# Kernel optimization log

Hardware: AMD Instinct MI355X
Metric: run time of the kernel (lower is better)

The kernel has to match this reference:

```python
import jax, jax.numpy as jnp
import numpy as np

L1, L2, N, C = 4096, 4096, 8, 3


def setup_inputs() -> dict:
    key = jax.random.key(0)
    k1, k2 = jax.random.split(key)
    coords1 = jax.random.uniform(k1, (L1, N, C), dtype=jnp.float32)
    coords2 = jax.random.uniform(k2, (L2, N, C), dtype=jnp.float32)
    return {"coords1": coords1, "coords2": coords2}


def reference(coords1, coords2):
    # coords1: [L1, N, C], coords2: [L2, N, C]
    l1, n, c = coords1.shape
    l2 = coords2.shape[0]
    # Batch-first layout, matching flatten_batch semantics (per-batch NN only)
    q = jnp.swapaxes(coords2, 0, 1)  # [N, L2, C] query points
    r = jnp.swapaxes(coords1, 0, 1)  # [N, L1, C] reference points
    # Squared euclidean distances per batch: [N, L2, L1]
    d2 = (
        jnp.sum(q * q, axis=-1)[:, :, None]
        + jnp.sum(r * r, axis=-1)[:, None, :]
        - 2.0 * jnp.einsum("nlc,nmc->nlm", q, r)
    )
    # tc.nearest returns global flat index; original does fmod(L1) to get the
    # per-batch index — argmin within each batch gives that directly.
    nearest = jnp.argmin(d2, axis=-1)  # [N, L2]
    clusters = nearest.T  # [L2, N]
    # torch.meshgrid(arange(L2), arange(N)) with 'ij' indexing; indices[-1] is
    # the batch index broadcast to [L2, N].
    batch_idx = jnp.broadcast_to(jnp.arange(n, dtype=jnp.int64 if False else jnp.int32), (l2, n))
    return (clusters.reshape(-1), batch_idx.reshape(-1))
```

## Files before the change

kernel.cpp:

```cpp
#include <hip/hip_runtime.h>
#include <float.h>


typedef float v2f __attribute__((ext_vector_type(2)));

constexpr int kL1 = 4096, kL2 = 4096, kN = 8;
constexpr int kChunk = 1024;
constexpr int kQPerBlock = 16;
constexpr int kQ = 4;

__device__ __forceinline__ v2f pk_mul(v2f a, v2f b) {
  v2f d; asm("v_pk_mul_f32 %0, %1, %2" : "=v"(d) : "v"(a), "v"(b)); return d;
}
__device__ __forceinline__ v2f pk_add(v2f a, v2f b) {
  v2f d; asm("v_pk_add_f32 %0, %1, %2" : "=v"(d) : "v"(a), "v"(b)); return d;
}
__device__ __forceinline__ v2f pk_fma(v2f a, v2f b, v2f c) {
  v2f d; asm("v_pk_fma_f32 %0, %1, %2, %3" : "=v"(d) : "v"(a), "v"(b), "v"(c)); return d;
}

__device__ __forceinline__ v2f dist2_pair(v2f qx, v2f qy, v2f qz, v2f qq,
                                          v2f rx, v2f ry, v2f rz, v2f rr, v2f n2) {
  const v2f s01 = pk_add(pk_mul(qx, rx), pk_mul(qy, ry));
  const v2f dot = pk_add(s01, pk_mul(qz, rz));
  const v2f A = pk_add(qq, rr);
  return pk_fma(dot, n2, A);
}

__global__ __launch_bounds__(256, 4)
void nearest_kernel(const float* __restrict__ c1, const float* __restrict__ c2,
                    int* __restrict__ out) {
#pragma clang fp contract(off)
  __shared__ float sRx[kChunk], sRy[kChunk], sRz[kChunk], sRr[kChunk];

  const int tid = threadIdx.x;
  const int n = blockIdx.y;
  const int wave = tid >> 6;
  const int lane = tid & 63;
  const int q0 = blockIdx.x * kQPerBlock + wave * kQ;

  float qxs[kQ], qys[kQ], qzs[kQ], qqs[kQ];
  v2f qx2[kQ], qy2[kQ], qz2[kQ], qq2[kQ];
#pragma unroll
  for (int i = 0; i < kQ; ++i) {
    const float* p = c2 + ((q0 + i) * kN + n) * 3;
    qxs[i] = p[0]; qys[i] = p[1]; qzs[i] = p[2];
    qqs[i] = __fadd_rn(__fadd_rn(__fmul_rn(qxs[i], qxs[i]), __fmul_rn(qys[i], qys[i])),
                       __fmul_rn(qzs[i], qzs[i]));
    qx2[i] = (v2f){qxs[i], qxs[i]};
    qy2[i] = (v2f){qys[i], qys[i]};
    qz2[i] = (v2f){qzs[i], qzs[i]};
    qq2[i] = (v2f){qqs[i], qqs[i]};
  }
  const v2f n2 = {-2.0f, -2.0f};

  float bd[kQ]; int bt[kQ];
#pragma unroll
  for (int i = 0; i < kQ; ++i) { bd[i] = FLT_MAX; bt[i] = 0; }

  for (int chunk = 0; chunk < kL1 / kChunk; ++chunk) {
    __syncthreads();

    {
      const int jb = chunk * kChunk + tid * 4;
      float x[4], y[4], z[4], w4[4];
#pragma unroll
      for (int k = 0; k < 4; ++k) {
        const float* p = c1 + ((jb + k) * kN + n) * 3;
        x[k] = p[0]; y[k] = p[1]; z[k] = p[2];
        w4[k] = __fadd_rn(__fadd_rn(__fmul_rn(x[k], x[k]), __fmul_rn(y[k], y[k])),
                          __fmul_rn(z[k], z[k]));
      }
      *reinterpret_cast<float4*>(&sRx[tid * 4]) = make_float4(x[0], x[1], x[2], x[3]);
      *reinterpret_cast<float4*>(&sRy[tid * 4]) = make_float4(y[0], y[1], y[2], y[3]);
      *reinterpret_cast<float4*>(&sRz[tid * 4]) = make_float4(z[0], z[1], z[2], z[3]);
      *reinterpret_cast<float4*>(&sRr[tid * 4]) = make_float4(w4[0], w4[1], w4[2], w4[3]);
    }
    __syncthreads();

#pragma unroll
    for (int t = 0; t < kChunk / 256; ++t) {
      const int tg = chunk * (kChunk / 256) + t;
      const int base = t * 256 + lane * 4;
      const float4 rx4 = *reinterpret_cast<const float4*>(&sRx[base]);
      const float4 ry4 = *reinterpret_cast<const float4*>(&sRy[base]);
      const float4 rz4 = *reinterpret_cast<const float4*>(&sRz[base]);
      const float4 rr4 = *reinterpret_cast<const float4*>(&sRr[base]);
      const v2f rx01 = {rx4.x, rx4.y}, rx23 = {rx4.z, rx4.w};
      const v2f ry01 = {ry4.x, ry4.y}, ry23 = {ry4.z, ry4.w};
      const v2f rz01 = {rz4.x, rz4.y}, rz23 = {rz4.z, rz4.w};
      const v2f rr01 = {rr4.x, rr4.y}, rr23 = {rr4.z, rr4.w};

#pragma unroll
      for (int i = 0; i < kQ; ++i) {
        const v2f d01 = dist2_pair(qx2[i], qy2[i], qz2[i], qq2[i],
                                   rx01, ry01, rz01, rr01, n2);
        const v2f d23 = dist2_pair(qx2[i], qy2[i], qz2[i], qq2[i],
                                   rx23, ry23, rz23, rr23, n2);
        const float old = bd[i];
        float m = fminf(fminf(d01.x, d01.y), old);
        m = fminf(fminf(d23.x, d23.y), m);
        bd[i] = m;
        if (m < old) bt[i] = tg;
      }
    }
  }

  int sel[kQ];
#pragma unroll
  for (int i = 0; i < kQ; ++i) sel[i] = bt[i] * 64 + lane;
#pragma unroll
  for (int m = 1; m <= 32; m <<= 1) {
#pragma unroll
    for (int i = 0; i < kQ; ++i) {
      const float od = __shfl_xor(bd[i], m);
      const int os = __shfl_xor(sel[i], m);
      if (od < bd[i] || (od == bd[i] && os < sel[i])) { bd[i] = od; sel[i] = os; }
    }
  }

#pragma unroll
  for (int i = 0; i < kQ; ++i) {
    if (lane == i) {
      const int j0 = sel[i] * 4;
      float best = FLT_MAX; int kk = 0;
#pragma unroll
      for (int k = 0; k < 4; ++k) {
        const float* p = c1 + ((j0 + k) * kN + n) * 3;
        const float r0 = p[0], r1 = p[1], r2 = p[2];
        const float rr = __fadd_rn(
            __fadd_rn(__fmul_rn(r0, r0), __fmul_rn(r1, r1)), __fmul_rn(r2, r2));
        const float dot = __fadd_rn(
            __fadd_rn(__fmul_rn(qxs[i], r0), __fmul_rn(qys[i], r1)),
            __fmul_rn(qzs[i], r2));
        const float dc = __fmaf_rn(-2.0f, dot, __fadd_rn(qqs[i], rr));
        if (dc < best) { best = dc; kk = k; }
      }
      out[(q0 + i) * kN + n] = j0 + kk;
      out[kL2 * kN + (q0 + i) * kN + n] = n;
    }
  }
}

extern "C" void kernel_launch(void* const* d_in, const int* in_sizes, int n_in,
                              void* d_out, int out_size, void* d_ws, size_t ws_size,
                              hipStream_t stream) {
  const float* c1 = (const float*)d_in[0];
  const float* c2 = (const float*)d_in[1];
  int* out = (int*)d_out;
  dim3 grid(kL2 / kQPerBlock, kN);
  nearest_kernel<<<grid, dim3(256), 0, stream>>>(c1, c2, out);
}
```

Baseline: 99.80 us.

## Precompute SoA reference layout in workspace and read it directly from global memory

Adds a pre-pass kernel that transposes coords1 into per-batch SoA arrays (x, y, z, |r|^2) in the workspace. The main kernel then streams these arrays from global/L2 with float4 loads, with no LDS staging or __syncthreads. Both paths also replace the inline-asm packed FP32 math with scalar arithmetic. This removes the strided AoS gathers that every block repeated and the block barriers, at the cost of an extra kernel launch, workspace traffic, and losing the packed-math throughput.

```diff
diff --git a/kernel.cpp b/kernel.cpp
--- a/kernel.cpp
+++ b/kernel.cpp
@@ -2,37 +2,126 @@
 #include <float.h>
 
 
-typedef float v2f __attribute__((ext_vector_type(2)));
-
 constexpr int kL1 = 4096, kL2 = 4096, kN = 8;
-constexpr int kChunk = 1024;
 constexpr int kQPerBlock = 16;
 constexpr int kQ = 4;
-
-__device__ __forceinline__ v2f pk_mul(v2f a, v2f b) {
-  v2f d; asm("v_pk_mul_f32 %0, %1, %2" : "=v"(d) : "v"(a), "v"(b)); return d;
-}
-__device__ __forceinline__ v2f pk_add(v2f a, v2f b) {
-  v2f d; asm("v_pk_add_f32 %0, %1, %2" : "=v"(d) : "v"(a), "v"(b)); return d;
-}
-__device__ __forceinline__ v2f pk_fma(v2f a, v2f b, v2f c) {
-  v2f d; asm("v_pk_fma_f32 %0, %1, %2, %3" : "=v"(d) : "v"(a), "v"(b), "v"(c)); return d;
-}
-
-__device__ __forceinline__ v2f dist2_pair(v2f qx, v2f qy, v2f qz, v2f qq,
-                                          v2f rx, v2f ry, v2f rz, v2f rr, v2f n2) {
-  const v2f s01 = pk_add(pk_mul(qx, rx), pk_mul(qy, ry));
-  const v2f dot = pk_add(s01, pk_mul(qz, rz));
-  const v2f A = pk_add(qq, rr);
-  return pk_fma(dot, n2, A);
+constexpr int kSoAFloats = kN * kL1;
+constexpr size_t kWsBytes = 4ull * kSoAFloats * sizeof(float);
+
+__global__ __launch_bounds__(256)
+void soa_kernel(const float* __restrict__ c1, float* __restrict__ ws) {
+#pragma clang fp contract(off)
+  const int t = blockIdx.x * 256 + threadIdx.x;
+  const int n = t & (kN - 1);
+  const int j = t >> 3;
+  const float* p = c1 + t * 3;
+  const float x = p[0], y = p[1], z = p[2];
+  const float rr = __fadd_rn(
+      __fadd_rn(__fmul_rn(x, x), __fmul_rn(y, y)), __fmul_rn(z, z));
+  const int o = n * kL1 + j;
+  ws[o] = x;
+  ws[kSoAFloats + o] = y;
+  ws[2 * kSoAFloats + o] = z;
+  ws[3 * kSoAFloats + o] = rr;
 }
 
 __global__ __launch_bounds__(256, 4)
-void nearest_kernel(const float* __restrict__ c1, const float* __restrict__ c2,
-                    int* __restrict__ out) {
+void nearest_soa_kernel(const float* __restrict__ ws, const float* __restrict__ c2,
+                        int* __restrict__ out) {
+#pragma clang fp contract(off)
+  const int n = blockIdx.y;
+  const int wave = threadIdx.x >> 6;
+  const int lane = threadIdx.x & 63;
+  const int q0 = blockIdx.x * kQPerBlock + wave * kQ;
+
+  const float* __restrict__ X = ws + n * kL1;
+  const float* __restrict__ Y = ws + kSoAFloats + n * kL1;
+  const float* __restrict__ Z = ws + 2 * kSoAFloats + n * kL1;
+  const float* __restrict__ RR = ws + 3 * kSoAFloats + n * kL1;
+
+  float qx[kQ], qy[kQ], qz[kQ], qq[kQ];
+#pragma unroll
+  for (int i = 0; i < kQ; ++i) {
+    const float* p = c2 + ((q0 + i) * kN + n) * 3;
+    qx[i] = p[0]; qy[i] = p[1]; qz[i] = p[2];
+    qq[i] = __fadd_rn(__fadd_rn(__fmul_rn(qx[i], qx[i]), __fmul_rn(qy[i], qy[i])),
+                      __fmul_rn(qz[i], qz[i]));
+  }
+
+  float bd[kQ]; int bt[kQ];
+#pragma unroll
+  for (int i = 0; i < kQ; ++i) { bd[i] = FLT_MAX; bt[i] = 0; }
+
+#pragma unroll 2
+  for (int t = 0; t < kL1 / 256; ++t) {
+    const int b = t * 256 + lane * 4;
+    const float4 x4 = *reinterpret_cast<const float4*>(X + b);
+    const float4 y4 = *reinterpret_cast<const float4*>(Y + b);
+    const float4 z4 = *reinterpret_cast<const float4*>(Z + b);
+    const float4 r4 = *reinterpret_cast<const float4*>(RR + b);
+    const float xs[4] = {x4.x, x4.y, x4.z, x4.w};
+    const float ys[4] = {y4.x, y4.y, y4.z, y4.w};
+    const float zs[4] = {z4.x, z4.y, z4.z, z4.w};
+    const float rs[4] = {r4.x, r4.y, r4.z, r4.w};
+
+#pragma unroll
+    for (int i = 0; i < kQ; ++i) {
+      float d[4];
+#pragma unroll
+      for (int k = 0; k < 4; ++k) {
+        const float dot = __fadd_rn(
+            __fadd_rn(__fmul_rn(qx[i], xs[k]), __fmul_rn(qy[i], ys[k])),
+            __fmul_rn(qz[i], zs[k]));
+        d[k] = __fmaf_rn(-2.0f, dot, __fadd_rn(qq[i], rs[k]));
+      }
+      const float old = bd[i];
+      float m = fminf(fminf(d[0], d[1]), old);
+      m = fminf(fminf(d[2], d[3]), m);
+      bd[i] = m;
+      if (m < old) bt[i] = t;
+    }
+  }
+
+  int sel[kQ];
+#pragma unroll
+  for (int i = 0; i < kQ; ++i) sel[i] = bt[i] * 64 + lane;
+#pragma unroll
+  for (int m = 1; m <= 32; m <<= 1) {
+#pragma unroll
+    for (int i = 0; i < kQ; ++i) {
+      const float od = __shfl_xor(bd[i], m);
+      const int os = __shfl_xor(sel[i], m);
+      if (od < bd[i] || (od == bd[i] && os < sel[i])) { bd[i] = od; sel[i] = os; }
+    }
+  }
+
+#pragma unroll
+  for (int i = 0; i < kQ; ++i) {
+    if (lane == i) {
+      const int j0 = sel[i] * 4;
+      float best = FLT_MAX; int kk = 0;
+#pragma unroll
+      for (int k = 0; k < 4; ++k) {
+        const float dot = __fadd_rn(
+            __fadd_rn(__fmul_rn(qx[i], X[j0 + k]), __fmul_rn(qy[i], Y[j0 + k])),
+            __fmul_rn(qz[i], Z[j0 + k]));
+        const float dc = __fmaf_rn(-2.0f, dot, __fadd_rn(qq[i], RR[j0 + k]));
+        if (dc < best) { best = dc; kk = k; }
+      }
+      out[(q0 + i) * kN + n] = j0 + kk;
+      out[kL2 * kN + (q0 + i) * kN + n] = n;
+    }
+  }
+}
+
+typedef float v2f __attribute__((ext_vector_type(2)));
+constexpr int kChunk = 1024;
+
+__global__ __launch_bounds__(256, 4)
+void nearest_kernel_lds(const float* __restrict__ c1, const float* __restrict__ c2,
+                        int* __restrict__ out) {
 #pragma clang fp contract(off)
   __shared__ float sRx[kChunk], sRy[kChunk], sRz[kChunk], sRr[kChunk];
-
   const int tid = threadIdx.x;
   const int n = blockIdx.y;
   const int wave = tid >> 6;
@@ -40,19 +129,13 @@
   const int q0 = blockIdx.x * kQPerBlock + wave * kQ;
 
   float qxs[kQ], qys[kQ], qzs[kQ], qqs[kQ];
-  v2f qx2[kQ], qy2[kQ], qz2[kQ], qq2[kQ];
 #pragma unroll
   for (int i = 0; i < kQ; ++i) {
     const float* p = c2 + ((q0 + i) * kN + n) * 3;
     qxs[i] = p[0]; qys[i] = p[1]; qzs[i] = p[2];
     qqs[i] = __fadd_rn(__fadd_rn(__fmul_rn(qxs[i], qxs[i]), __fmul_rn(qys[i], qys[i])),
                        __fmul_rn(qzs[i], qzs[i]));
-    qx2[i] = (v2f){qxs[i], qxs[i]};
-    qy2[i] = (v2f){qys[i], qys[i]};
-    qz2[i] = (v2f){qzs[i], qzs[i]};
-    qq2[i] = (v2f){qqs[i], qqs[i]};
-  }
-  const v2f n2 = {-2.0f, -2.0f};
+  }
 
   float bd[kQ]; int bt[kQ];
 #pragma unroll
@@ -60,7 +143,6 @@
 
   for (int chunk = 0; chunk < kL1 / kChunk; ++chunk) {
     __syncthreads();
-
     {
       const int jb = chunk * kChunk + tid * 4;
       float x[4], y[4], z[4], w4[4];
@@ -82,24 +164,27 @@
     for (int t = 0; t < kChunk / 256; ++t) {
       const int tg = chunk * (kChunk / 256) + t;
       const int base = t * 256 + lane * 4;
-      const float4 rx4 = *reinterpret_cast<const float4*>(&sRx[base]);
-      const float4 ry4 = *reinterpret_cast<const float4*>(&sRy[base]);
-      const float4 rz4 = *reinterpret_cast<const float4*>(&sRz[base]);
-      const float4 rr4 = *reinterpret_cast<const float4*>(&sRr[base]);
-      const v2f rx01 = {rx4.x, rx4.y}, rx23 = {rx4.z, rx4.w};
-      const v2f ry01 = {ry4.x, ry4.y}, ry23 = {ry4.z, ry4.w};
-      const v2f rz01 = {rz4.x, rz4.y}, rz23 = {rz4.z, rz4.w};
-      const v2f rr01 = {rr4.x, rr4.y}, rr23 = {rr4.z, rr4.w};
-
+      const float4 x4 = *reinterpret_cast<const float4*>(&sRx[base]);
+      const float4 y4 = *reinterpret_cast<const float4*>(&sRy[base]);
+      const float4 z4 = *reinterpret_cast<const float4*>(&sRz[base]);
+      const float4 r4 = *reinterpret_cast<const float4*>(&sRr[base]);
+      const float xs[4] = {x4.x, x4.y, x4.z, x4.w};
+      const float ys[4] = {y4.x, y4.y, y4.z, y4.w};
+      const float zs[4] = {z4.x, z4.y, z4.z, z4.w};
+      const float rs[4] = {r4.x, r4.y, r4.z, r4.w};
 #pragma unroll
       for (int i = 0; i < kQ; ++i) {
-        const v2f d01 = dist2_pair(qx2[i], qy2[i], qz2[i], qq2[i],
-                                   rx01, ry01, rz01, rr01, n2);
-        const v2f d23 = dist2_pair(qx2[i], qy2[i], qz2[i], qq2[i],
-                                   rx23, ry23, rz23, rr23, n2);
+        float d[4];
+#pragma unroll
+        for (int k = 0; k < 4; ++k) {
+          const float dot = __fadd_rn(
+              __fadd_rn(__fmul_rn(qxs[i], xs[k]), __fmul_rn(qys[i], ys[k])),
+              __fmul_rn(qzs[i], zs[k]));
+          d[k] = __fmaf_rn(-2.0f, dot, __fadd_rn(qqs[i], rs[k]));
+        }
         const float old = bd[i];
-        float m = fminf(fminf(d01.x, d01.y), old);
-        m = fminf(fminf(d23.x, d23.y), m);
+        float m = fminf(fminf(d[0], d[1]), old);
+        m = fminf(fminf(d[2], d[3]), m);
         bd[i] = m;
         if (m < old) bt[i] = tg;
       }
@@ -148,6 +233,13 @@
   const float* c1 = (const float*)d_in[0];
   const float* c2 = (const float*)d_in[1];
   int* out = (int*)d_out;
-  dim3 grid(kL2 / kQPerBlock, kN);
-  nearest_kernel<<<grid, dim3(256), 0, stream>>>(c1, c2, out);
-}
+  if (d_ws != nullptr && ws_size >= kWsBytes) {
+    float* ws = (float*)d_ws;
+    soa_kernel<<<dim3(kL1 * kN / 256), dim3(256), 0, stream>>>(c1, ws);
+    dim3 grid(kL2 / kQPerBlock, kN);
+    nearest_soa_kernel<<<grid, dim3(256), 0, stream>>>(ws, c2, out);
+  } else {
+    dim3 grid(kL2 / kQPerBlock, kN);
+    nearest_kernel_lds<<<grid, dim3(256), 0, stream>>>(c1, c2, out);
+  }
+}
```

Result: faster. 90.07 us (-9.7%).

## Replace brute-force nearest search with uniform-grid binning and ring search

Applied to the files above, without the earlier changes.

Adds a binning kernel that sorts reference points per batch into an 8x8x8 uniform grid in workspace, storing precomputed squared norms and original indices. A second kernel assigns 8 lanes to each query and searches expanding shells of cells, stopping early once the shell distance bound exceeds the current best. This replaces O(L1) distance evaluations per query with a local search, at the cost of an extra launch, atomics, and divergence. The grid assumes coordinates lie in [0,1], which is only true for the uniform test distribution. Points outside that range are clamped into edge cells, so the pruning bound may not hold for other inputs. If no workspace is provided it falls back to the old brute-force kernel, now written with scalar ops.

```diff
diff --git a/kernel.cpp b/kernel.cpp
--- a/kernel.cpp
+++ b/kernel.cpp
@@ -2,37 +2,152 @@
 #include <float.h>
 
 
-typedef float v2f __attribute__((ext_vector_type(2)));
-
 constexpr int kL1 = 4096, kL2 = 4096, kN = 8;
-constexpr int kChunk = 1024;
+constexpr int kCS = 520;
+constexpr size_t kOffPts = 8ull * kCS * 4;
+constexpr size_t kOffIdx = kOffPts + 8ull * kL1 * 16;
+constexpr size_t kWsBytes = kOffIdx + 8ull * kL1 * 4;
+
+__device__ __forceinline__ float rr_exact(float x, float y, float z) {
+  return __fadd_rn(__fadd_rn(__fmul_rn(x, x), __fmul_rn(y, y)), __fmul_rn(z, z));
+}
+
+__global__ __launch_bounds__(1024)
+void bin_kernel(const float* __restrict__ c1, int* __restrict__ cellStart,
+                float4* __restrict__ pts, int* __restrict__ pidx) {
+#pragma clang fp contract(off)
+  __shared__ int cnt[512];
+  const int tid = threadIdx.x;
+  const int n = blockIdx.x;
+  if (tid < 512) cnt[tid] = 0;
+  __syncthreads();
+
+  float xs[4], ys[4], zs[4];
+  int cl[4];
+#pragma unroll
+  for (int k = 0; k < 4; ++k) {
+    const int j = k * 1024 + tid;
+    const float* p = c1 + (j * kN + n) * 3;
+    const float x = p[0], y = p[1], z = p[2];
+    xs[k] = x; ys[k] = y; zs[k] = z;
+    const int cx = min(7, max(0, (int)(x * 8.0f)));
+    const int cy = min(7, max(0, (int)(y * 8.0f)));
+    const int cz = min(7, max(0, (int)(z * 8.0f)));
+    cl[k] = (cz * 8 + cy) * 8 + cx;
+    atomicAdd(&cnt[cl[k]], 1);
+  }
+  __syncthreads();
+
+  if (tid < 64) {
+    int loc[8], part = 0;
+#pragma unroll
+    for (int i = 0; i < 8; ++i) { loc[i] = cnt[tid * 8 + i]; part += loc[i]; }
+    int inc = part;
+#pragma unroll
+    for (int off = 1; off < 64; off <<= 1) {
+      const int v = __shfl_up(inc, off);
+      if (tid >= off) inc += v;
+    }
+    int base = inc - part;
+#pragma unroll
+    for (int i = 0; i < 8; ++i) {
+      const int c = tid * 8 + i;
+      cellStart[n * kCS + c] = base;
+      cnt[c] = base;
+      base += loc[i];
+    }
+    if (tid == 0) cellStart[n * kCS + 512] = kL1;
+  }
+  __syncthreads();
+
+#pragma unroll
+  for (int k = 0; k < 4; ++k) {
+    const int j = k * 1024 + tid;
+    const int pos = atomicAdd(&cnt[cl[k]], 1);
+    pts[n * kL1 + pos] = make_float4(xs[k], ys[k], zs[k], rr_exact(xs[k], ys[k], zs[k]));
+    pidx[n * kL1 + pos] = j;
+  }
+}
+
+__global__ __launch_bounds__(256, 8)
+void grid_nn_kernel(const int* __restrict__ cellStart, const float4* __restrict__ pts,
+                    const int* __restrict__ pidx, const float* __restrict__ c2,
+                    int* __restrict__ out) {
+#pragma clang fp contract(off)
+  const int gid = blockIdx.x * 256 + threadIdx.x;
+  const int query = gid >> 3;
+  const int sub = gid & 7;
+  const int qj = query >> 3;
+  const int n = query & 7;
+
+  const float* p = c2 + (qj * kN + n) * 3;
+  const float qx = p[0], qy = p[1], qz = p[2];
+  const float qq = rr_exact(qx, qy, qz);
+  const int cx = min(7, max(0, (int)(qx * 8.0f)));
+  const int cy = min(7, max(0, (int)(qy * 8.0f)));
+  const int cz = min(7, max(0, (int)(qz * 8.0f)));
+
+  const int* __restrict__ cs = cellStart + n * kCS;
+  const float4* __restrict__ P = pts + n * kL1;
+  const int* __restrict__ I = pidx + n * kL1;
+
+  float bd = FLT_MAX;
+  int bi = 0x7FFFFFFF;
+
+  for (int r = 0; r < 8; ++r) {
+    if (r > 0) {
+      const float t = (r - 1) * 0.125f;
+      if (t * t > __fadd_rn(bd, 4e-6f)) break;
+    }
+    for (int dz = -r; dz <= r; ++dz) {
+      const int z = cz + dz;
+      if (z < 0 || z > 7) continue;
+      const bool zf = (dz == r || dz == -r);
+      for (int dy = -r; dy <= r; ++dy) {
+        const int y = cy + dy;
+        if (y < 0 || y > 7) continue;
+        const bool zyf = zf || dy == r || dy == -r;
+        for (int dx = -r; dx <= r; ++dx) {
+          if (!zyf && dx != r && dx != -r) continue;
+          const int x = cx + dx;
+          if (x < 0 || x > 7) continue;
+          const int c = (z * 8 + y) * 8 + x;
+          const int s = cs[c], e = cs[c + 1];
+          for (int pp = s + sub; pp < e; pp += 8) {
+            const float4 rp = P[pp];
+            const int id = I[pp];
+            const float dot = __fadd_rn(
+                __fadd_rn(__fmul_rn(qx, rp.x), __fmul_rn(qy, rp.y)),
+                __fmul_rn(qz, rp.z));
+            const float d2 = __fmaf_rn(-2.0f, dot, __fadd_rn(qq, rp.w));
+            if (d2 < bd || (d2 == bd && id < bi)) { bd = d2; bi = id; }
+          }
+        }
+      }
+    }
+#pragma unroll
+    for (int m = 1; m <= 4; m <<= 1) {
+      const float od = __shfl_xor(bd, m);
+      const int oi = __shfl_xor(bi, m);
+      if (od < bd || (od == bd && oi < bi)) { bd = od; bi = oi; }
+    }
+  }
+
+  if (sub == 0) {
+    out[qj * kN + n] = bi;
+    out[kL2 * kN + qj * kN + n] = n;
+  }
+}
+
 constexpr int kQPerBlock = 16;
 constexpr int kQ = 4;
-
-__device__ __forceinline__ v2f pk_mul(v2f a, v2f b) {
-  v2f d; asm("v_pk_mul_f32 %0, %1, %2" : "=v"(d) : "v"(a), "v"(b)); return d;
-}
-__device__ __forceinline__ v2f pk_add(v2f a, v2f b) {
-  v2f d; asm("v_pk_add_f32 %0, %1, %2" : "=v"(d) : "v"(a), "v"(b)); return d;
-}
-__device__ __forceinline__ v2f pk_fma(v2f a, v2f b, v2f c) {
-  v2f d; asm("v_pk_fma_f32 %0, %1, %2, %3" : "=v"(d) : "v"(a), "v"(b), "v"(c)); return d;
-}
-
-__device__ __forceinline__ v2f dist2_pair(v2f qx, v2f qy, v2f qz, v2f qq,
-                                          v2f rx, v2f ry, v2f rz, v2f rr, v2f n2) {
-  const v2f s01 = pk_add(pk_mul(qx, rx), pk_mul(qy, ry));
-  const v2f dot = pk_add(s01, pk_mul(qz, rz));
-  const v2f A = pk_add(qq, rr);
-  return pk_fma(dot, n2, A);
-}
+constexpr int kChunk = 1024;
 
 __global__ __launch_bounds__(256, 4)
-void nearest_kernel(const float* __restrict__ c1, const float* __restrict__ c2,
-                    int* __restrict__ out) {
+void nearest_kernel_lds(const float* __restrict__ c1, const float* __restrict__ c2,
+                        int* __restrict__ out) {
 #pragma clang fp contract(off)
   __shared__ float sRx[kChunk], sRy[kChunk], sRz[kChunk], sRr[kChunk];
-
   const int tid = threadIdx.x;
   const int n = blockIdx.y;
   const int wave = tid >> 6;
@@ -40,27 +155,18 @@
   const int q0 = blockIdx.x * kQPerBlock + wave * kQ;
 
   float qxs[kQ], qys[kQ], qzs[kQ], qqs[kQ];
-  v2f qx2[kQ], qy2[kQ], qz2[kQ], qq2[kQ];
 #pragma unroll
   for (int i = 0; i < kQ; ++i) {
     const float* p = c2 + ((q0 + i) * kN + n) * 3;
     qxs[i] = p[0]; qys[i] = p[1]; qzs[i] = p[2];
-    qqs[i] = __fadd_rn(__fadd_rn(__fmul_rn(qxs[i], qxs[i]), __fmul_rn(qys[i], qys[i])),
-                       __fmul_rn(qzs[i], qzs[i]));
-    qx2[i] = (v2f){qxs[i], qxs[i]};
-    qy2[i] = (v2f){qys[i], qys[i]};
-    qz2[i] = (v2f){qzs[i], qzs[i]};
-    qq2[i] = (v2f){qqs[i], qqs[i]};
-  }
-  const v2f n2 = {-2.0f, -2.0f};
-
+    qqs[i] = rr_exact(qxs[i], qys[i], qzs[i]);
+  }
   float bd[kQ]; int bt[kQ];
 #pragma unroll
   for (int i = 0; i < kQ; ++i) { bd[i] = FLT_MAX; bt[i] = 0; }
 
   for (int chunk = 0; chunk < kL1 / kChunk; ++chunk) {
     __syncthreads();
-
     {
       const int jb = chunk * kChunk + tid * 4;
       float x[4], y[4], z[4], w4[4];
@@ -68,8 +174,7 @@
       for (int k = 0; k < 4; ++k) {
         const float* p = c1 + ((jb + k) * kN + n) * 3;
         x[k] = p[0]; y[k] = p[1]; z[k] = p[2];
-        w4[k] = __fadd_rn(__fadd_rn(__fmul_rn(x[k], x[k]), __fmul_rn(y[k], y[k])),
-                          __fmul_rn(z[k], z[k]));
+        w4[k] = rr_exact(x[k], y[k], z[k]);
       }
       *reinterpret_cast<float4*>(&sRx[tid * 4]) = make_float4(x[0], x[1], x[2], x[3]);
       *reinterpret_cast<float4*>(&sRy[tid * 4]) = make_float4(y[0], y[1], y[2], y[3]);
@@ -77,35 +182,36 @@
       *reinterpret_cast<float4*>(&sRr[tid * 4]) = make_float4(w4[0], w4[1], w4[2], w4[3]);
     }
     __syncthreads();
-
 #pragma unroll
     for (int t = 0; t < kChunk / 256; ++t) {
       const int tg = chunk * (kChunk / 256) + t;
       const int base = t * 256 + lane * 4;
-      const float4 rx4 = *reinterpret_cast<const float4*>(&sRx[base]);
-      const float4 ry4 = *reinterpret_cast<const float4*>(&sRy[base]);
-      const float4 rz4 = *reinterpret_cast<const float4*>(&sRz[base]);
-      const float4 rr4 = *reinterpret_cast<const float4*>(&sRr[base]);
-      const v2f rx01 = {rx4.x, rx4.y}, rx23 = {rx4.z, rx4.w};
-      const v2f ry01 = {ry4.x, ry4.y}, ry23 = {ry4.z, ry4.w};
-      const v2f rz01 = {rz4.x, rz4.y}, rz23 = {rz4.z, rz4.w};
-      const v2f rr01 = {rr4.x, rr4.y}, rr23 = {rr4.z, rr4.w};
-
+      const float4 x4 = *reinterpret_cast<const float4*>(&sRx[base]);
+      const float4 y4 = *reinterpret_cast<const float4*>(&sRy[base]);
+      const float4 z4 = *reinterpret_cast<const float4*>(&sRz[base]);
+      const float4 r4 = *reinterpret_cast<const float4*>(&sRr[base]);
+      const float xs[4] = {x4.x, x4.y, x4.z, x4.w};
+      const float ys[4] = {y4.x, y4.y, y4.z, y4.w};
+      const float zs[4] = {z4.x, z4.y, z4.z, z4.w};
+      const float rs[4] = {r4.x, r4.y, r4.z, r4.w};
 #pragma unroll
       for (int i = 0; i < kQ; ++i) {
-        const v2f d01 = dist2_pair(qx2[i], qy2[i], qz2[i], qq2[i],
-                                   rx01, ry01, rz01, rr01, n2);
-        const v2f d23 = dist2_pair(qx2[i], qy2[i], qz2[i], qq2[i],
-                                   rx23, ry23, rz23, rr23, n2);
+        float d[4];
+#pragma unroll
+        for (int k = 0; k < 4; ++k) {
+          const float dot = __fadd_rn(
+              __fadd_rn(__fmul_rn(qxs[i], xs[k]), __fmul_rn(qys[i], ys[k])),
+              __fmul_rn(qzs[i], zs[k]));
+          d[k] = __fmaf_rn(-2.0f, dot, __fadd_rn(qqs[i], rs[k]));
+        }
         const float old = bd[i];
-        float m = fminf(fminf(d01.x, d01.y), old);
-        m = fminf(fminf(d23.x, d23.y), m);
+        float m = fminf(fminf(d[0], d[1]), old);
+        m = fminf(fminf(d[2], d[3]), m);
         bd[i] = m;
         if (m < old) bt[i] = tg;
       }
     }
   }
-
   int sel[kQ];
 #pragma unroll
   for (int i = 0; i < kQ; ++i) sel[i] = bt[i] * 64 + lane;
@@ -118,7 +224,6 @@
       if (od < bd[i] || (od == bd[i] && os < sel[i])) { bd[i] = od; sel[i] = os; }
     }
   }
-
 #pragma unroll
   for (int i = 0; i < kQ; ++i) {
     if (lane == i) {
@@ -128,8 +233,7 @@
       for (int k = 0; k < 4; ++k) {
         const float* p = c1 + ((j0 + k) * kN + n) * 3;
         const float r0 = p[0], r1 = p[1], r2 = p[2];
-        const float rr = __fadd_rn(
-            __fadd_rn(__fmul_rn(r0, r0), __fmul_rn(r1, r1)), __fmul_rn(r2, r2));
+        const float rr = rr_exact(r0, r1, r2);
         const float dot = __fadd_rn(
             __fadd_rn(__fmul_rn(qxs[i], r0), __fmul_rn(qys[i], r1)),
             __fmul_rn(qzs[i], r2));
@@ -148,6 +252,15 @@
   const float* c1 = (const float*)d_in[0];
   const float* c2 = (const float*)d_in[1];
   int* out = (int*)d_out;
-  dim3 grid(kL2 / kQPerBlock, kN);
-  nearest_kernel<<<grid, dim3(256), 0, stream>>>(c1, c2, out);
-}
+  if (d_ws != nullptr && ws_size >= kWsBytes) {
+    int* cellStart = (int*)d_ws;
+    float4* pts = (float4*)((char*)d_ws + kOffPts);
+    int* pidx = (int*)((char*)d_ws + kOffIdx);
+    bin_kernel<<<dim3(kN), dim3(1024), 0, stream>>>(c1, cellStart, pts, pidx);
+    grid_nn_kernel<<<dim3(kL2 * kN * 8 / 256), dim3(256), 0, stream>>>(
+        cellStart, pts, pidx, c2, out);
+  } else {
+    dim3 grid(kL2 / kQPerBlock, kN);
+    nearest_kernel_lds<<<grid, dim3(256), 0, stream>>>(c1, c2, out);
+  }
+}
```

Result: faster. 85.88 us (-14.0%).
